# Optimization experiments

Hardware: AMD Instinct MI355X
Metric: run time of the kernel (lower is better)

The kernel has to match this reference:

```python
import jax, jax.numpy as jnp
import numpy as np

N_HEADS = 16
HEAD_SZ = 64

def setup_inputs() -> dict:
    key = jax.random.key(0)
    ks = jax.random.split(key, 6)
    E = 1024
    s = 1.0 / np.sqrt(E)
    return {
        "x": jax.random.normal(ks[0], (2, 2048, E), dtype=jnp.float32),
        "Wq": jax.random.normal(ks[1], (E, N_HEADS * HEAD_SZ), dtype=jnp.float32) * s,
        "Wk": jax.random.normal(ks[2], (E, N_HEADS * HEAD_SZ), dtype=jnp.float32) * s,
        "Wv": jax.random.normal(ks[3], (E, N_HEADS * HEAD_SZ), dtype=jnp.float32) * s,
        "Wp": jax.random.normal(ks[4], (N_HEADS * HEAD_SZ, E), dtype=jnp.float32) * s,
        "bp": jnp.zeros((E,), dtype=jnp.float32),
    }

def reference(x, Wq, Wk, Wv, Wp, bp):
    # flavor="masked": causal self-attention, pdrop=0 -> dropout is identity
    B, S, E = x.shape
    H, D = N_HEADS, HEAD_SZ
    q = (x @ Wq).reshape(B, S, H, D).transpose(0, 2, 1, 3)  # [B,H,S,D]
    k = (x @ Wk).reshape(B, S, H, D).transpose(0, 2, 1, 3)
    v = (x @ Wv).reshape(B, S, H, D).transpose(0, 2, 1, 3)
    scores = jnp.einsum("bhqd,bhkd->bhqk", q, k) / jnp.sqrt(jnp.float32(D))
    causal = jnp.tril(jnp.ones((S, S), dtype=bool))  # [S,S]
    scores = jnp.where(causal, scores, -jnp.inf)
    attn = jax.nn.softmax(scores, axis=-1)
    out = jnp.einsum("bhqk,bhkd->bhqd", attn, v)  # [B,H,S,D]
    out = out.transpose(0, 2, 1, 3).reshape(B, S, H * D)
    return out @ Wp + bp
```

## Files before the change

kernel.cpp:

```cpp
#include <hip/hip_runtime.h>
#include <hip/hip_bf16.h>
#include <math.h>

using bf16 = __hip_bfloat16;
typedef __attribute__((ext_vector_type(8))) short short8;
typedef __attribute__((ext_vector_type(4))) float floatx4;

#define MFMA16(a, b, c) __builtin_amdgcn_mfma_f32_16x16x32_bf16((a), (b), (c), 0, 0, 0)

__device__ __forceinline__ void gll16(const void* g, void* l) {
  __builtin_amdgcn_global_load_lds((__attribute__((address_space(1))) void*)(uintptr_t)g,
                                   (__attribute__((address_space(3))) void*)l, 16, 0, 0);
}

__global__ void detect_bias_k(const unsigned short* __restrict__ x,
                              const void* __restrict__ bsrc,
                              bf16* __restrict__ bdst, int* __restrict__ flag) {
  __shared__ int cnt;
  if (threadIdx.x == 0) cnt = 0;
  __syncthreads();
  int local = 0;
  for (int i = threadIdx.x; i < 8192; i += 256) {
    unsigned short v = x[2 * i];
    if (((v >> 7) & 0xFF) == 0xFF) local++;
  }
  if (local) atomicAdd(&cnt, local);
  __syncthreads();
  int f = (cnt > 0) ? 1 : 0;
  if (threadIdx.x == 0) *flag = f;
  for (int i = threadIdx.x; i < 1024; i += 256)
    bdst[i] = f ? __float2bfloat16(((const float*)bsrc)[i]) : ((const bf16*)bsrc)[i];
}

__global__ __launch_bounds__(256) void prep_k(const void* __restrict__ xin,
                                              bf16* __restrict__ xb,
                                              const void* __restrict__ W0,
                                              const void* __restrict__ W1,
                                              const void* __restrict__ W2,
                                              const void* __restrict__ W3,
                                              bf16* __restrict__ Wt,
                                              bf16* __restrict__ Wpt,
                                              const int* __restrict__ flag) {
  bool f32 = (*flag != 0);
  int z = blockIdx.z;
  if (z < 2) {
    int tid = threadIdx.y * 32 + threadIdx.x;
    int blockLin = z * 1024 + blockIdx.y * 32 + blockIdx.x;
    int idx = blockLin * 2048 + tid * 8;
    if (f32) {
      const float4* p = reinterpret_cast<const float4*>((const float*)xin + idx);
      float4 a = p[0], b = p[1];
      union { bf16 h[8]; uint4 u; } U;
      U.h[0] = __float2bfloat16(a.x); U.h[1] = __float2bfloat16(a.y);
      U.h[2] = __float2bfloat16(a.z); U.h[3] = __float2bfloat16(a.w);
      U.h[4] = __float2bfloat16(b.x); U.h[5] = __float2bfloat16(b.y);
      U.h[6] = __float2bfloat16(b.z); U.h[7] = __float2bfloat16(b.w);
      *reinterpret_cast<uint4*>(xb + idx) = U.u;
    } else {
      *reinterpret_cast<uint4*>(xb + idx) =
          *reinterpret_cast<const uint4*>((const bf16*)xin + idx);
    }
    return;
  }
  const void* src = (z == 2) ? W0 : (z == 3) ? W1 : (z == 4) ? W2 : W3;
  bf16* dst = (z == 5) ? Wpt : (Wt + (size_t)(z - 2) * 1024 * 1024);
  __shared__ float tsh[32][33];
  int tx = threadIdx.x, ty = threadIdx.y;
  int k0 = blockIdx.y * 32, n0 = blockIdx.x * 32;
  for (int i = 0; i < 4; i++) {
    size_t off = (size_t)(k0 + ty + i * 8) * 1024 + n0 + tx;
    tsh[ty + i * 8][tx] = f32 ? ((const float*)src)[off]
                              : __bfloat162float(((const bf16*)src)[off]);
  }
  __syncthreads();
  for (int i = 0; i < 4; i++)
    dst[(size_t)(n0 + ty + i * 8) * 1024 + k0 + tx] = __float2bfloat16(tsh[tx][ty + i * 8]);
}

__global__ __launch_bounds__(512) void vtrans_k(const bf16* __restrict__ QKV,
                                                bf16* __restrict__ VT) {
  __shared__ bf16 t[64][66];
  int tx = threadIdx.x, ty = threadIdx.y;
  int s0 = blockIdx.x * 64, bh = blockIdx.y;
  int b = bh >> 4, h = bh & 15;
  size_t rowb = (size_t)b * 2048;
  int hv = 2048 + h * 64;
#pragma unroll
  for (int i = 0; i < 8; i++)
    t[i * 8 + ty][tx] = QKV[(rowb + s0 + i * 8 + ty) * 3072 + hv + tx];
  __syncthreads();
#pragma unroll
  for (int i = 0; i < 8; i++)
    VT[((size_t)bh * 64 + i * 8 + ty) * 2048 + s0 + tx] = t[tx][i * 8 + ty];
}

__global__ __launch_bounds__(256) void gemm_bt128(const bf16* __restrict__ A, int lda,
                                                  const bf16* __restrict__ Bt, int ldb,
                                                  void* __restrict__ C, int ldc,
                                                  const bf16* __restrict__ bias, int K,
                                                  const int* __restrict__ outflag) {
  __shared__ bf16 As[2][128 * 32];
  __shared__ bf16 Bs[2][128 * 32];
  int t = threadIdx.x;
  int w = t >> 6, lane = t & 63;
  int g = lane >> 4, c = lane & 15;
  int wm = (w >> 1) * 64, wn = (w & 1) * 64;
  int m0 = blockIdx.y * 128, n0 = blockIdx.x * 128;

  int sr = w * 32 + (lane >> 2);
  int sc = (lane & 3) * 8;
  const bf16* Ab = A + (size_t)(m0 + sr) * lda + sc;
  const bf16* Bb = Bt + (size_t)(n0 + sr) * ldb + sc;
  int lofs = (w * 32) * 32;

  floatx4 acc[4][4] = {};

  for (int k0 = 0; k0 < K; k0 += 64) {
    __syncthreads();
#pragma unroll
    for (int h = 0; h < 2; h++) {
      gll16(Ab + k0 + h * 32, &As[h][lofs]);
      gll16(Ab + k0 + h * 32 + (size_t)16 * lda, &As[h][lofs + 16 * 32]);
      gll16(Bb + k0 + h * 32, &Bs[h][lofs]);
      gll16(Bb + k0 + h * 32 + (size_t)16 * ldb, &Bs[h][lofs + 16 * 32]);
    }
    __syncthreads();
#pragma unroll
    for (int h = 0; h < 2; h++) {
      short8 af[4], bf[4];
#pragma unroll
      for (int i = 0; i < 4; i++) {
        af[i] = *reinterpret_cast<const short8*>(&As[h][(wm + i * 16 + c) * 32 + g * 8]);
        bf[i] = *reinterpret_cast<const short8*>(&Bs[h][(wn + i * 16 + c) * 32 + g * 8]);
      }
#pragma unroll
      for (int i = 0; i < 4; i++)
#pragma unroll
        for (int j = 0; j < 4; j++) acc[i][j] = MFMA16(af[i], bf[j], acc[i][j]);
    }
  }

  bool f32out = (outflag != nullptr) && (*outflag != 0);
#pragma unroll
  for (int i = 0; i < 4; i++) {
    int rbase = m0 + wm + i * 16 + g * 4;
#pragma unroll
    for (int j = 0; j < 4; j++) {
      int col = n0 + wn + j * 16 + c;
      float bv = bias ? __bfloat162float(bias[col]) : 0.f;
#pragma unroll
      for (int r = 0; r < 4; r++) {
        size_t off = (size_t)(rbase + r) * ldc + col;
        float v = acc[i][j][r] + bv;
        if (f32out) ((float*)C)[off] = v;
        else ((bf16*)C)[off] = __float2bfloat16(v);
      }
    }
  }
}

__global__ __launch_bounds__(256) void gemm_bt64(const bf16* __restrict__ A, int lda,
                                                 const bf16* __restrict__ Bt, int ldb,
                                                 void* __restrict__ C, int ldc,
                                                 const bf16* __restrict__ bias, int K,
                                                 const int* __restrict__ outflag) {
  __shared__ bf16 As[2][128 * 32];
  __shared__ bf16 Bs[2][64 * 32];
  int t = threadIdx.x;
  int w = t >> 6, lane = t & 63;
  int g = lane >> 4, c = lane & 15;
  int wm = (w >> 1) * 64, wn = (w & 1) * 32;
  int m0 = blockIdx.y * 128, n0 = blockIdx.x * 64;

  int sr = (lane >> 2);
  int sc = (lane & 3) * 8;
  const bf16* Ab = A + (size_t)(m0 + w * 32 + sr) * lda + sc;
  const bf16* Bb = Bt + (size_t)(n0 + w * 16 + sr) * ldb + sc;
  int laofs = (w * 32) * 32;
  int lbofs = (w * 16) * 32;

  floatx4 acc[4][2] = {};

  for (int k0 = 0; k0 < K; k0 += 64) {
    __syncthreads();
#pragma unroll
    for (int h = 0; h < 2; h++) {
      gll16(Ab + k0 + h * 32, &As[h][laofs]);
      gll16(Ab + k0 + h * 32 + (size_t)16 * lda, &As[h][laofs + 16 * 32]);
      gll16(Bb + k0 + h * 32, &Bs[h][lbofs]);
    }
    __syncthreads();
#pragma unroll
    for (int h = 0; h < 2; h++) {
      short8 af[4], bf[2];
#pragma unroll
      for (int i = 0; i < 4; i++)
        af[i] = *reinterpret_cast<const short8*>(&As[h][(wm + i * 16 + c) * 32 + g * 8]);
#pragma unroll
      for (int j = 0; j < 2; j++)
        bf[j] = *reinterpret_cast<const short8*>(&Bs[h][(wn + j * 16 + c) * 32 + g * 8]);
#pragma unroll
      for (int i = 0; i < 4; i++)
#pragma unroll
        for (int j = 0; j < 2; j++) acc[i][j] = MFMA16(af[i], bf[j], acc[i][j]);
    }
  }

  bool f32out = (outflag != nullptr) && (*outflag != 0);
#pragma unroll
  for (int i = 0; i < 4; i++) {
    int rbase = m0 + wm + i * 16 + g * 4;
#pragma unroll
    for (int j = 0; j < 2; j++) {
      int col = n0 + wn + j * 16 + c;
      float bv = bias ? __bfloat162float(bias[col]) : 0.f;
#pragma unroll
      for (int r = 0; r < 4; r++) {
        size_t off = (size_t)(rbase + r) * ldc + col;
        float v = acc[i][j][r] + bv;
        if (f32out) ((float*)C)[off] = v;
        else ((bf16*)C)[off] = __float2bfloat16(v);
      }
    }
  }
}

__global__ __launch_bounds__(512, 4) void attn_lds2(bf16* __restrict__ QKV,
                                                    const bf16* __restrict__ VT) {
  const int S = 2048, LD = 3072;
  __shared__ bf16 Ks[2][2][64 * 32];
  __shared__ bf16 Vs[2][2][64 * 32];
  __shared__ bf16 Pb[8][16 * 72];

  int t = threadIdx.x, w = t >> 6, lane = t & 63, g = lane >> 4, c = lane & 15;

  int r = blockIdx.x + 16 * blockIdx.y;
  int xcd = r & 7;
  int s = r >> 3;
  int m = s >> 4;
  int u = s & 15;
  int bh = xcd + 8 * m;
  int qt = (m & 2) ? (15 - u) : u;

  int b = bh >> 4, h = bh & 15;
  int qbase = qt * 128;
  size_t rowb = (size_t)b * S;
  int hq = h * 64, hk = 1024 + h * 64;
  const bf16* Vt = VT + (size_t)bh * 64 * 2048;
  bf16* pb = Pb[w];

  int su = (w & 3) * 16 + (lane >> 2);
  int sc = (lane & 3) * 8;
  const bf16* Kg = &QKV[(rowb + su) * LD + hk + sc];
  const bf16* Vg = &Vt[(size_t)su * 2048 + sc];
  int sofs = ((w & 3) * 16) * 32;

  short8 qf[2];
#pragma unroll
  for (int hf = 0; hf < 2; hf++)
    qf[hf] = *reinterpret_cast<const short8*>(
        &QKV[(rowb + qbase + w * 16 + c) * LD + hq + hf * 32 + g * 8]);

  floatx4 o[4] = {};
  float lsum = 0.f;
  int qrow = qbase + w * 16 + c;

  int nkt = 2 * qt + 2;
  if (w < 4) {
    gll16(Kg, &Ks[0][0][sofs]);
    gll16(Kg + 32, &Ks[0][1][sofs]);
  } else {
    gll16(Vg, &Vs[0][0][sofs]);
    gll16(Vg + 32, &Vs[0][1][sofs]);
  }

  for (int kt = 0; kt < nkt; kt++) {
    int kbase = kt * 64;
    int cur = kt & 1;
    __syncthreads();
    if (kt + 1 < nkt) {
      int nb = cur ^ 1;
      size_t kofs = (size_t)(kbase + 64);
      if (w < 4) {
        gll16(Kg + kofs * LD, &Ks[nb][0][sofs]);
        gll16(Kg + kofs * LD + 32, &Ks[nb][1][sofs]);
      } else {
        gll16(Vg + kofs, &Vs[nb][0][sofs]);
        gll16(Vg + kofs + 32, &Vs[nb][1][sofs]);
      }
    }

    short8 kf[4][2];
#pragma unroll
    for (int nt = 0; nt < 4; nt++)
#pragma unroll
      for (int hf = 0; hf < 2; hf++)
        kf[nt][hf] =
            *reinterpret_cast<const short8*>(&Ks[cur][hf][(nt * 16 + c) * 32 + g * 8]);

    floatx4 sv[4];
    __builtin_amdgcn_s_setprio(1);
#pragma unroll
    for (int nt = 0; nt < 4; nt++) {
      floatx4 z = {};
      z = MFMA16(kf[nt][0], qf[0], z);
      z = MFMA16(kf[nt][1], qf[1], z);
      sv[nt] = z;
    }
    __builtin_amdgcn_s_setprio(0);

    bool diag = (kbase + 63 > qbase + w * 16);
#pragma unroll
    for (int nt = 0; nt < 4; nt++) {
      int kcol0 = kbase + nt * 16 + g * 4;
#pragma unroll
      for (int rr = 0; rr < 4; rr++) {
        float arg = fmaf(sv[nt][rr], 0.18033688f, -23.083120f);
        if (diag && (kcol0 + rr > qrow)) arg = -1e30f;
        float p = exp2f(arg);
        lsum += p;
        sv[nt][rr] = p;
      }
    }

#pragma unroll
    for (int nt = 0; nt < 4; nt++) {
      union { bf16 h4[4]; uint2 u2; } U;
      U.h4[0] = __float2bfloat16(sv[nt][0]);
      U.h4[1] = __float2bfloat16(sv[nt][1]);
      U.h4[2] = __float2bfloat16(sv[nt][2]);
      U.h4[3] = __float2bfloat16(sv[nt][3]);
      *reinterpret_cast<uint2*>(&pb[c * 72 + nt * 16 + g * 4]) = U.u2;
    }
    asm volatile("s_waitcnt lgkmcnt(0)" ::: "memory");
    short8 pf0 = *reinterpret_cast<const short8*>(&pb[c * 72 + g * 8]);
    short8 pf1 = *reinterpret_cast<const short8*>(&pb[c * 72 + 32 + g * 8]);

    __builtin_amdgcn_s_setprio(1);
#pragma unroll
    for (int dt = 0; dt < 4; dt++) {
      short8 vf0 = *reinterpret_cast<const short8*>(&Vs[cur][0][(dt * 16 + c) * 32 + g * 8]);
      short8 vf1 = *reinterpret_cast<const short8*>(&Vs[cur][1][(dt * 16 + c) * 32 + g * 8]);
      o[dt] = MFMA16(pf0, vf0, o[dt]);
      o[dt] = MFMA16(pf1, vf1, o[dt]);
    }
    __builtin_amdgcn_s_setprio(0);
  }

  lsum += __shfl_xor(lsum, 16);
  lsum += __shfl_xor(lsum, 32);
  float lrec = 1.0f / lsum;
  float l_r[4];
#pragma unroll
  for (int rr = 0; rr < 4; rr++) l_r[rr] = __shfl(lrec, g * 4 + rr);

#pragma unroll
  for (int dt = 0; dt < 4; dt++)
#pragma unroll
    for (int rr = 0; rr < 4; rr++) {
      float v = o[dt][rr] * l_r[rr];
      QKV[(rowb + qbase + w * 16 + g * 4 + rr) * LD + hq + dt * 16 + c] =
          __float2bfloat16(v);
    }
}

extern "C" void kernel_launch(void* const* d_in, const int* in_sizes, int n_in,
                              void* d_out, int out_size, void* d_ws, size_t ws_size,
                              hipStream_t stream) {
  char* ws = (char*)d_ws;
  const size_t MB = 1024 * 1024;
  int* flag = (int*)ws;
  bf16* bias = (bf16*)(ws + 4096);
  bf16* xb = (bf16*)(ws + 1 * MB);
  bf16* Wt = (bf16*)(ws + 9 * MB);
  bf16* Wpt = (bf16*)(ws + 15 * MB);
  bf16* QKV = (bf16*)(ws + 17 * MB);
  bf16* VT = xb;

  detect_bias_k<<<1, 256, 0, stream>>>((const unsigned short*)d_in[0], d_in[5], bias, flag);
  prep_k<<<dim3(32, 32, 6), dim3(32, 8), 0, stream>>>(d_in[0], xb, d_in[1], d_in[2],
                                                      d_in[3], d_in[4], Wt, Wpt, flag);

  gemm_bt128<<<dim3(24, 32), 256, 0, stream>>>(xb, 1024, Wt, 1024, QKV, 3072, nullptr,
                                               1024, nullptr);
  vtrans_k<<<dim3(32, 32), dim3(64, 8), 0, stream>>>(QKV, VT);
  attn_lds2<<<dim3(16, 32), 512, 0, stream>>>(QKV, VT);
  gemm_bt64<<<dim3(16, 32), 256, 0, stream>>>(QKV, 3072, Wpt, 1024, d_out, 1024, bias,
                                              1024, flag);
}
```

Measured before the change: 198.5 us.

## Halve attention query tile and load V fragments directly from global

The attention kernel now uses 64-query tiles with 4 waves per block instead of 128 queries with 8 waves, and launches twice as many blocks. V is no longer staged through LDS: each wave reads its V fragments straight from the transposed V buffer in global memory into registers, and only K stays double-buffered in LDS. This cuts LDS use and barrier traffic and gives finer causal load balance, at the cost of redundant global/L2 reads of V across waves and less K reuse per block.

```diff
diff --git a/kernel.cpp b/kernel.cpp
--- a/kernel.cpp
+++ b/kernel.cpp
@@ -225,35 +225,38 @@
   }
 }
 
-__global__ __launch_bounds__(512, 4) void attn_lds2(bf16* __restrict__ QKV,
+__global__ __launch_bounds__(256, 4) void attn_lds2(bf16* __restrict__ QKV,
                                                     const bf16* __restrict__ VT) {
   const int S = 2048, LD = 3072;
   __shared__ bf16 Ks[2][2][64 * 32];
-  __shared__ bf16 Vs[2][2][64 * 32];
-  __shared__ bf16 Pb[8][16 * 72];
+  __shared__ bf16 Pb[4][16 * 72];
 
   int t = threadIdx.x, w = t >> 6, lane = t & 63, g = lane >> 4, c = lane & 15;
 
-  int r = blockIdx.x + 16 * blockIdx.y;
+  int r = blockIdx.x + 32 * blockIdx.y;
   int xcd = r & 7;
   int s = r >> 3;
-  int m = s >> 4;
-  int u = s & 15;
+  int m = s >> 5;
+  int u = s & 31;
   int bh = xcd + 8 * m;
-  int qt = (m & 2) ? (15 - u) : u;
+  int qt = (m & 2) ? (31 - u) : u;
 
   int b = bh >> 4, h = bh & 15;
-  int qbase = qt * 128;
+  int qbase = qt * 64;
   size_t rowb = (size_t)b * S;
   int hq = h * 64, hk = 1024 + h * 64;
   const bf16* Vt = VT + (size_t)bh * 64 * 2048;
   bf16* pb = Pb[w];
 
-  int su = (w & 3) * 16 + (lane >> 2);
+  int su = w * 16 + (lane >> 2);
   int sc = (lane & 3) * 8;
   const bf16* Kg = &QKV[(rowb + su) * LD + hk + sc];
-  const bf16* Vg = &Vt[(size_t)su * 2048 + sc];
-  int sofs = ((w & 3) * 16) * 32;
+  int sofs = (w * 16) * 32;
+
+  const bf16* Vr[4];
+#pragma unroll
+  for (int dt = 0; dt < 4; dt++)
+    Vr[dt] = Vt + (size_t)(dt * 16 + c) * 2048 + g * 8;
 
   short8 qf[2];
 #pragma unroll
@@ -265,14 +268,9 @@
   float lsum = 0.f;
   int qrow = qbase + w * 16 + c;
 
-  int nkt = 2 * qt + 2;
-  if (w < 4) {
-    gll16(Kg, &Ks[0][0][sofs]);
-    gll16(Kg + 32, &Ks[0][1][sofs]);
-  } else {
-    gll16(Vg, &Vs[0][0][sofs]);
-    gll16(Vg + 32, &Vs[0][1][sofs]);
-  }
+  int nkt = qt + 1;
+  gll16(Kg, &Ks[0][0][sofs]);
+  gll16(Kg + 32, &Ks[0][1][sofs]);
 
   for (int kt = 0; kt < nkt; kt++) {
     int kbase = kt * 64;
@@ -281,13 +279,8 @@
     if (kt + 1 < nkt) {
       int nb = cur ^ 1;
       size_t kofs = (size_t)(kbase + 64);
-      if (w < 4) {
-        gll16(Kg + kofs * LD, &Ks[nb][0][sofs]);
-        gll16(Kg + kofs * LD + 32, &Ks[nb][1][sofs]);
-      } else {
-        gll16(Vg + kofs, &Vs[nb][0][sofs]);
-        gll16(Vg + kofs + 32, &Vs[nb][1][sofs]);
-      }
+      gll16(Kg + kofs * LD, &Ks[nb][0][sofs]);
+      gll16(Kg + kofs * LD + 32, &Ks[nb][1][sofs]);
     }
 
     short8 kf[4][2];
@@ -323,6 +316,13 @@
       }
     }
 
+    short8 vf0[4], vf1[4];
+#pragma unroll
+    for (int dt = 0; dt < 4; dt++) {
+      vf0[dt] = *reinterpret_cast<const short8*>(Vr[dt] + kbase);
+      vf1[dt] = *reinterpret_cast<const short8*>(Vr[dt] + kbase + 32);
+    }
+
 #pragma unroll
     for (int nt = 0; nt < 4; nt++) {
       union { bf16 h4[4]; uint2 u2; } U;
@@ -339,10 +339,8 @@
     __builtin_amdgcn_s_setprio(1);
 #pragma unroll
     for (int dt = 0; dt < 4; dt++) {
-      short8 vf0 = *reinterpret_cast<const short8*>(&Vs[cur][0][(dt * 16 + c) * 32 + g * 8]);
-      short8 vf1 = *reinterpret_cast<const short8*>(&Vs[cur][1][(dt * 16 + c) * 32 + g * 8]);
-      o[dt] = MFMA16(pf0, vf0, o[dt]);
-      o[dt] = MFMA16(pf1, vf1, o[dt]);
+      o[dt] = MFMA16(pf0, vf0[dt], o[dt]);
+      o[dt] = MFMA16(pf1, vf1[dt], o[dt]);
     }
     __builtin_amdgcn_s_setprio(0);
   }
@@ -384,7 +382,7 @@
   gemm_bt128<<<dim3(24, 32), 256, 0, stream>>>(xb, 1024, Wt, 1024, QKV, 3072, nullptr,
                                                1024, nullptr);
   vtrans_k<<<dim3(32, 32), dim3(64, 8), 0, stream>>>(QKV, VT);
-  attn_lds2<<<dim3(16, 32), 512, 0, stream>>>(QKV, VT);
+  attn_lds2<<<dim3(32, 32), 256, 0, stream>>>(QKV, VT);
   gemm_bt64<<<dim3(16, 32), 256, 0, stream>>>(QKV, 3072, Wpt, 1024, d_out, 1024, bias,
                                               1024, flag);
 }
```

Measured after the change: 237.9 us. 1.2x slower.

## Replace QKV projection GEMM with double-buffered 256x256-tile kernel

Applied to the files above, without the earlier changes.

Replaces the 128x128-tile QKV GEMM with a 512-thread kernel that computes 256x256 output tiles. It double-buffers the LDS stages so global-to-LDS loads for the next K step overlap MFMA work on the current one, using an explicit vmcnt wait and barriers. It also raises wave priority around the MFMA block. The larger tile increases data reuse per LDS load, but it cuts the grid to 192 blocks, fewer than the CU count. It also uses about 128KB of LDS per block, which limits occupancy.

```diff
diff --git a/kernel.cpp b/kernel.cpp
--- a/kernel.cpp
+++ b/kernel.cpp
@@ -94,69 +94,81 @@
     VT[((size_t)bh * 64 + i * 8 + ty) * 2048 + s0 + tx] = t[tx][i * 8 + ty];
 }
 
-__global__ __launch_bounds__(256) void gemm_bt128(const bf16* __restrict__ A, int lda,
+__global__ __launch_bounds__(512, 2) void gemm256(const bf16* __restrict__ A, int lda,
                                                   const bf16* __restrict__ Bt, int ldb,
-                                                  void* __restrict__ C, int ldc,
-                                                  const bf16* __restrict__ bias, int K,
-                                                  const int* __restrict__ outflag) {
-  __shared__ bf16 As[2][128 * 32];
-  __shared__ bf16 Bs[2][128 * 32];
-  int t = threadIdx.x;
-  int w = t >> 6, lane = t & 63;
-  int g = lane >> 4, c = lane & 15;
-  int wm = (w >> 1) * 64, wn = (w & 1) * 64;
-  int m0 = blockIdx.y * 128, n0 = blockIdx.x * 128;
-
-  int sr = w * 32 + (lane >> 2);
-  int sc = (lane & 3) * 8;
-  const bf16* Ab = A + (size_t)(m0 + sr) * lda + sc;
-  const bf16* Bb = Bt + (size_t)(n0 + sr) * ldb + sc;
-  int lofs = (w * 32) * 32;
-
-  floatx4 acc[4][4] = {};
-
-  for (int k0 = 0; k0 < K; k0 += 64) {
-    __syncthreads();
-#pragma unroll
-    for (int h = 0; h < 2; h++) {
-      gll16(Ab + k0 + h * 32, &As[h][lofs]);
-      gll16(Ab + k0 + h * 32 + (size_t)16 * lda, &As[h][lofs + 16 * 32]);
-      gll16(Bb + k0 + h * 32, &Bs[h][lofs]);
-      gll16(Bb + k0 + h * 32 + (size_t)16 * ldb, &Bs[h][lofs + 16 * 32]);
-    }
-    __syncthreads();
-#pragma unroll
-    for (int h = 0; h < 2; h++) {
-      short8 af[4], bf[4];
-#pragma unroll
-      for (int i = 0; i < 4; i++) {
-        af[i] = *reinterpret_cast<const short8*>(&As[h][(wm + i * 16 + c) * 32 + g * 8]);
-        bf[i] = *reinterpret_cast<const short8*>(&Bs[h][(wn + i * 16 + c) * 32 + g * 8]);
-      }
-#pragma unroll
-      for (int i = 0; i < 4; i++)
-#pragma unroll
-        for (int j = 0; j < 4; j++) acc[i][j] = MFMA16(af[i], bf[j], acc[i][j]);
-    }
-  }
-
-  bool f32out = (outflag != nullptr) && (*outflag != 0);
-#pragma unroll
-  for (int i = 0; i < 4; i++) {
-    int rbase = m0 + wm + i * 16 + g * 4;
-#pragma unroll
-    for (int j = 0; j < 4; j++) {
-      int col = n0 + wn + j * 16 + c;
-      float bv = bias ? __bfloat162float(bias[col]) : 0.f;
-#pragma unroll
-      for (int r = 0; r < 4; r++) {
-        size_t off = (size_t)(rbase + r) * ldc + col;
-        float v = acc[i][j][r] + bv;
-        if (f32out) ((float*)C)[off] = v;
-        else ((bf16*)C)[off] = __float2bfloat16(v);
-      }
-    }
-  }
+                                                  bf16* __restrict__ C, int ldc, int K) {
+  __shared__ bf16 As[2][2][256 * 32];
+  __shared__ bf16 Bs[2][2][256 * 32];
+  int t = threadIdx.x, w = t >> 6, lane = t & 63, g = lane >> 4, c = lane & 15;
+  int wr = w >> 2, wc = w & 3;
+  int m0 = blockIdx.y * 256, n0 = blockIdx.x * 256;
+
+  int srow = w * 16 + (lane >> 2);
+  int scol = (lane & 3) * 8;
+  const bf16* Ab = A + (size_t)m0 * lda;
+  const bf16* Bb = Bt + (size_t)n0 * ldb;
+  int lofs = (w * 16) * 32;
+
+#define STAGE256(d, kk)                                                              \
+  {                                                                                  \
+    _Pragma("unroll") for (int rh = 0; rh < 2; rh++) {                               \
+      _Pragma("unroll") for (int kh = 0; kh < 2; kh++) {                             \
+        gll16(Ab + (size_t)(rh * 128 + srow) * lda + (kk) + kh * 32 + scol,          \
+              &As[d][kh][rh * 128 * 32 + lofs]);                                     \
+        gll16(Bb + (size_t)(rh * 128 + srow) * ldb + (kk) + kh * 32 + scol,          \
+              &Bs[d][kh][rh * 128 * 32 + lofs]);                                     \
+      }                                                                              \
+    }                                                                                \
+  }
+
+  floatx4 acc[8][4] = {};
+
+#define COMPUTE256(d)                                                                \
+  {                                                                                  \
+    _Pragma("unroll") for (int kh = 0; kh < 2; kh++) {                               \
+      short8 af[8], bfv[4];                                                          \
+      _Pragma("unroll") for (int mi = 0; mi < 8; mi++)                               \
+          af[mi] = *reinterpret_cast<const short8*>(                                 \
+              &As[d][kh][(wr * 128 + mi * 16 + c) * 32 + g * 8]);                    \
+      _Pragma("unroll") for (int ni = 0; ni < 4; ni++)                               \
+          bfv[ni] = *reinterpret_cast<const short8*>(                                \
+              &Bs[d][kh][(wc * 64 + ni * 16 + c) * 32 + g * 8]);                     \
+      __builtin_amdgcn_s_setprio(1);                                                 \
+      _Pragma("unroll") for (int mi = 0; mi < 8; mi++)                               \
+          _Pragma("unroll") for (int ni = 0; ni < 4; ni++)                           \
+              acc[mi][ni] = MFMA16(af[mi], bfv[ni], acc[mi][ni]);                    \
+      __builtin_amdgcn_s_setprio(0);                                                 \
+    }                                                                                \
+  }
+
+  int nt = K >> 6;
+  STAGE256(0, 0);
+  int cur = 0;
+  for (int tt = 0; tt < nt - 1; ++tt) {
+    STAGE256(cur ^ 1, (tt + 1) << 6);
+    asm volatile("s_waitcnt vmcnt(8)" ::: "memory");
+    asm volatile("s_barrier" ::: "memory");
+    COMPUTE256(cur);
+    asm volatile("s_barrier" ::: "memory");
+    cur ^= 1;
+  }
+  asm volatile("s_waitcnt vmcnt(0)" ::: "memory");
+  asm volatile("s_barrier" ::: "memory");
+  COMPUTE256(cur);
+
+#pragma unroll
+  for (int mi = 0; mi < 8; mi++) {
+    int row = m0 + wr * 128 + mi * 16 + g * 4;
+#pragma unroll
+    for (int ni = 0; ni < 4; ni++) {
+      int col = n0 + wc * 64 + ni * 16 + c;
+#pragma unroll
+      for (int r = 0; r < 4; r++)
+        C[(size_t)(row + r) * ldc + col] = __float2bfloat16(acc[mi][ni][r]);
+    }
+  }
+#undef STAGE256
+#undef COMPUTE256
 }
 
 __global__ __launch_bounds__(256) void gemm_bt64(const bf16* __restrict__ A, int lda,
@@ -381,8 +393,7 @@
   prep_k<<<dim3(32, 32, 6), dim3(32, 8), 0, stream>>>(d_in[0], xb, d_in[1], d_in[2],
                                                       d_in[3], d_in[4], Wt, Wpt, flag);
 
-  gemm_bt128<<<dim3(24, 32), 256, 0, stream>>>(xb, 1024, Wt, 1024, QKV, 3072, nullptr,
-                                               1024, nullptr);
+  gemm256<<<dim3(12, 16), 512, 0, stream>>>(xb, 1024, Wt, 1024, QKV, 3072, 1024);
   vtrans_k<<<dim3(32, 32), dim3(64, 8), 0, stream>>>(QKV, VT);
   attn_lds2<<<dim3(16, 32), 512, 0, stream>>>(QKV, VT);
   gemm_bt64<<<dim3(16, 32), 256, 0, stream>>>(QKV, 3072, Wpt, 1024, d_out, 1024, bias,
```

Result: slower. 209.9 us (+5.8%).
